# Kernel optimization log

Measured on AMD Instinct MI355X. Metric: run time of the kernel, lower is better.

The kernel has to match this reference:

```python
import jax, jax.numpy as jnp
import numpy as np

DT = 0.001
HIDDEN = 512
OUT = 128

def setup_inputs() -> dict:
    key = jax.random.key(0)
    k1, k2 = jax.random.split(key)
    x = jax.random.normal(k1, (64, 2048, HIDDEN), dtype=jnp.float32)
    # torch Linear default init ~ U(-1/sqrt(fan_in), 1/sqrt(fan_in)), weight shape [out, in]
    lim = 1.0 / np.sqrt(HIDDEN)
    W = jax.random.uniform(k2, (OUT, HIDDEN), dtype=jnp.float32, minval=-lim, maxval=lim)
    tau_syn = jnp.asarray(0.5, dtype=jnp.float32)  # tau_syn_out (used as tau_syn_inv)
    tau_mem = jnp.asarray(0.5, dtype=jnp.float32)  # tau_mem_out (used as tau_mem_inv)
    return {"x": x, "W": W, "tau_syn": tau_syn, "tau_mem": tau_mem}

def reference(x, W, tau_syn, tau_mem):
    # SNNDecode.forward: clamp taus, permute to [seq, batch, in], per-step
    # Linear + norse LI (leaky integrator) feed-forward step with v_leak = 0.
    tau_syn = jnp.clip(tau_syn, 0.0, 1.0)
    tau_mem = jnp.clip(tau_mem, 0.0, 1.0)
    batch, seq, _ = x.shape
    # The per-step Linear is recurrence-independent: hoist it into one big GEMM.
    # z_all: [seq, batch, out]
    z_all = jnp.einsum('bsh,oh->sbo', x, W)
    v0 = jnp.zeros((batch, OUT), dtype=x.dtype)
    i0 = jnp.zeros((batch, OUT), dtype=x.dtype)

    def step(carry, z):
        v, i = carry
        # li_feed_forward_step: dv = dt*tau_mem_inv*((v_leak - v) + i)
        v_new = v + DT * tau_mem * (i - v)
        i_dec = i - DT * tau_syn * i
        i_new = i_dec + z
        return (v_new, i_new), v_new

    (v_f, i_f), voltages = jax.lax.scan(step, (v0, i0), z_all)
    # output stacked over time: [seq, batch, out]; final state (v, i)
    return voltages, v_f, i_f
```

## Files before the change

kernel.cpp:

```cpp
#include <hip/hip_runtime.h>
#include <hip/hip_bf16.h>


typedef __attribute__((ext_vector_type(4))) float          f4;
typedef __attribute__((ext_vector_type(8))) short          s8;
typedef __attribute__((ext_vector_type(4))) unsigned       u4;
typedef __attribute__((ext_vector_type(4))) unsigned short su4;

#define SEQ    2048
#define HID    512
#define CHAINS 8192
#define VOLT   16777216
#define NCH    64
#define CHUNK  32

__device__ __forceinline__ float clamp01(float x) { return fminf(fmaxf(x, 0.f), 1.f); }

__device__ __forceinline__ unsigned pkbf(float x, float y) {
  float2 t; t.x = x; t.y = y;
  union { __hip_bfloat162 h; unsigned u; } c;
  c.h = __float22bfloat162_rn(t);
  return c.u;
}

__device__ __forceinline__ unsigned short f2bf(float f) {
  union { float f; unsigned u; } c; c.f = f;
  unsigned u = c.u;
  unsigned r = (u + 0x7fffu + ((u >> 16) & 1u)) >> 16;
  return (unsigned short)r;
}

__device__ __forceinline__ float bf2f(unsigned short s) {
  union { unsigned u; float f; } c; c.u = ((unsigned)s) << 16; return c.f;
}

__device__ __forceinline__ int swz(int row, int k) {
  return (row * 64 + k) ^ ((row & 7) << 3);
}

__device__ __forceinline__ int zidx(int row, int col) {
  return row * 128 + (col ^ (((row >> 2) & 7) << 4));
}

__global__ __launch_bounds__(256) void k_wconv(const float* __restrict__ W,
                                               unsigned short* __restrict__ Wb) {
  const int i = blockIdx.x * 256 + threadIdx.x;
  const f4 lo = ((const f4*)W)[2 * i];
  const f4 hi = ((const f4*)W)[2 * i + 1];
  su4 v0, v1;
#pragma unroll
  for (int j = 0; j < 4; ++j) { v0[j] = f2bf(lo[j]); v1[j] = f2bf(hi[j]); }
  ((su4*)Wb)[2 * i] = v0;
  ((su4*)Wb)[2 * i + 1] = v1;
}

template <int ZB>
__global__ __launch_bounds__(256, 2) void k_gemm(const float* __restrict__ X,
                                                 const unsigned short* __restrict__ Wb,
                                                 float* __restrict__ Out,
                                                 unsigned short* __restrict__ zbf,
                                                 const float* __restrict__ tau_syn,
                                                 const float* __restrict__ tau_mem,
                                                 float* __restrict__ ws) {
  __shared__ __align__(16) char smem[32768];
  short* const AS           = (short*)smem;
  unsigned short* const ZSb = (unsigned short*)smem;

  const int tid = threadIdx.x;
  const int blk = blockIdx.x;
  const int m0  = blk << 7;
  const int bI  = blk >> 4;
  const int t0  = (blk & 15) << 7;

  const int rbase = tid >> 3;
  const int coff  = (tid & 7) << 3;

  const int lane = tid & 63;
  const int wid  = tid >> 6;
  const int wmb  = (wid >> 1) << 6;
  const int wnb  = (wid & 1) << 6;
  const int lr   = lane & 15;
  const int lk   = (lane >> 4) << 3;

  const float* pX[4];
#pragma unroll
  for (int c = 0; c < 4; ++c)
    pX[c] = X + (size_t)(m0 + (c << 5) + rbase) * HID + coff;
  const unsigned short* pB[4];
#pragma unroll
  for (int ni = 0; ni < 4; ++ni)
    pB[ni] = Wb + (size_t)(wnb + (ni << 4) + lr) * HID + lk;

  f4 acc[4][4];
#pragma unroll
  for (int mi = 0; mi < 4; ++mi)
#pragma unroll
    for (int ni = 0; ni < 4; ++ni) acc[mi][ni] = (f4){0.f, 0.f, 0.f, 0.f};

  f4 xa[3][4][2];
#pragma unroll
  for (int c = 0; c < 4; ++c) {
    xa[0][c][0] = *(const f4*)(pX[c]);
    xa[0][c][1] = *(const f4*)(pX[c] + 4);
    xa[1][c][0] = *(const f4*)(pX[c] + 64);
    xa[1][c][1] = *(const f4*)(pX[c] + 68);
  }

#pragma unroll
  for (int ks = 0; ks < 8; ++ks) {
    const int cur = ks % 3;
    short* const Ac = AS + ((ks & 1) << 13);
#pragma unroll
    for (int c = 0; c < 4; ++c) {
      const int row = (c << 5) + rbase;
      u4 va;
      va[0] = pkbf(xa[cur][c][0][0], xa[cur][c][0][1]);
      va[1] = pkbf(xa[cur][c][0][2], xa[cur][c][0][3]);
      va[2] = pkbf(xa[cur][c][1][0], xa[cur][c][1][1]);
      va[3] = pkbf(xa[cur][c][1][2], xa[cur][c][1][3]);
      *(u4*)&Ac[swz(row, coff)] = va;
    }
    __syncthreads();
    s8 bg[2][4];
#pragma unroll
    for (int kk = 0; kk < 2; ++kk)
#pragma unroll
      for (int ni = 0; ni < 4; ++ni)
        bg[kk][ni] = *(const s8*)(pB[ni] + (ks << 6) + (kk << 5));
    if (ks < 6) {
      const int k0 = (ks + 2) << 6;
      const int nxt = (ks + 2) % 3;
#pragma unroll
      for (int c = 0; c < 4; ++c) {
        xa[nxt][c][0] = *(const f4*)(pX[c] + k0);
        xa[nxt][c][1] = *(const f4*)(pX[c] + k0 + 4);
      }
    }
#pragma unroll
    for (int kk = 0; kk < 2; ++kk) {
      s8 af[4];
#pragma unroll
      for (int mi = 0; mi < 4; ++mi)
        af[mi] = *(const s8*)&Ac[swz(wmb + (mi << 4) + lr, (kk << 5) + lk)];
#pragma unroll
      for (int mi = 0; mi < 4; ++mi)
#pragma unroll
        for (int ni = 0; ni < 4; ++ni)
          acc[mi][ni] = __builtin_amdgcn_mfma_f32_16x16x32_bf16(af[mi], bg[kk][ni],
                                                                acc[mi][ni], 0, 0, 0);
    }
  }

  __syncthreads();
  const int rr = (lane >> 4) << 2;
#pragma unroll
  for (int mi = 0; mi < 4; ++mi)
#pragma unroll
    for (int ni = 0; ni < 4; ++ni)
#pragma unroll
      for (int r = 0; r < 4; ++r)
        ZSb[zidx(wmb + (mi << 4) + rr + r, wnb + (ni << 4) + lr)] =
            f2bf(acc[mi][ni][r]);
  __syncthreads();

#pragma unroll
  for (int i = 0; i < 16; ++i) {
    const int idx  = (i << 8) + tid;
    const int toff = idx >> 5;
    const int c4   = idx & 31;
    const int colp = (c4 << 2) ^ (((toff >> 2) & 7) << 4);
    const su4 zb = *(const su4*)&ZSb[toff * 128 + colp];
    if (ZB) {
      *(su4*)(zbf + (size_t)(t0 + toff) * 8192 + (bI << 7) + (c4 << 2)) = zb;
    } else {
      f4 zf; zf[0] = bf2f(zb[0]); zf[1] = bf2f(zb[1]);
      zf[2] = bf2f(zb[2]); zf[3] = bf2f(zb[3]);
      *(f4*)(Out + (size_t)(t0 + toff) * 8192 + (bI << 7) + (c4 << 2)) = zf;
    }
  }
  {
    const float a  = 0.001f * clamp01(tau_mem[0]);
    const float eb = 1.f - 0.001f * clamp01(tau_syn[0]);
    const int col = tid & 127, h = tid >> 7;
    const int chain = (bI << 7) + col;
#pragma unroll
    for (int s = 0; s < 2; ++s) {
      const int r0 = (h << 6) + (s << 5);
      float v = 0.f, ii = 0.f;
#pragma unroll 8
      for (int j = 0; j < CHUNK; ++j) {
        const float z = bf2f(ZSb[zidx(r0 + j, col)]);
        v  = v + a * (ii - v);
        ii = eb * ii + z;
      }
      const int q = ((blk & 15) << 2) + (h << 1) + s;
      ws[q * CHAINS + chain]                 = v;
      ws[NCH * CHAINS + q * CHAINS + chain]  = ii;
    }
  }
}

__global__ __launch_bounds__(256) void k_comb(const float* __restrict__ tau_syn,
                                              const float* __restrict__ tau_mem,
                                              float* __restrict__ Out,
                                              float* __restrict__ ws) {
  __shared__ __align__(16) f4 SV[NCH][4], SI[NCH][4];
  const int tid = threadIdx.x;
  const int q   = tid >> 2;
  const int s   = tid & 3;
  const int cg  = blockIdx.x * 4 + s;
  const float a  = 0.001f * clamp01(tau_mem[0]);
  const float bb = 0.001f * clamp01(tau_syn[0]);
  const float ea = 1.f - a, eb = 1.f - bb;
  float P = 1.f, Q = 0.f, R = 1.f;
#pragma unroll
  for (int j = 0; j < CHUNK; ++j) { const float Pn = P * ea; Q = P * a + Q * eb; P = Pn; R *= eb; }

  f4* vend = (f4*)ws;
  f4* iend = vend + NCH * 2048;
  f4 xv = vend[q * 2048 + cg];
  f4 xi = iend[q * 2048 + cg];
  SV[q][s] = xv; SI[q][s] = xi;

  float Pd = P, Qd = Q, Rd = R;
#pragma unroll
  for (int d = 1; d < NCH; d <<= 1) {
    __syncthreads();
    f4 av, ai;
    const bool val = (q >= d);
    if (val) { av = SV[q - d][s]; ai = SI[q - d][s]; }
    __syncthreads();
    if (val) {
      xv = xv + Pd * av + Qd * ai;
      xi = xi + Rd * ai;
      SV[q][s] = xv; SI[q][s] = xi;
    }
    const float Pn = Pd * Pd;
    Qd = Pd * Qd + Qd * Rd;
    Pd = Pn;
    Rd = Rd * Rd;
  }
  __syncthreads();
  f4 iv = (f4){0.f, 0.f, 0.f, 0.f}, ij = (f4){0.f, 0.f, 0.f, 0.f};
  if (q > 0) { iv = SV[q - 1][s]; ij = SI[q - 1][s]; }
  vend[q * 2048 + cg] = iv;
  iend[q * 2048 + cg] = ij;
  if (q == NCH - 1) {
    ((f4*)(Out + VOLT))[cg]          = xv;
    ((f4*)(Out + VOLT + CHAINS))[cg] = xi;
  }
}

template <int ZB>
__global__ __launch_bounds__(256) void k_emit(const float* __restrict__ tau_syn,
                                              const float* __restrict__ tau_mem,
                                              float* __restrict__ Out,
                                              const unsigned short* __restrict__ zbf,
                                              const float* __restrict__ ws) {
  const int tid = threadIdx.x;
  const int cg = (blockIdx.x & 31) * 64 + (tid & 63);
  const int q  = (blockIdx.x >> 5) * 4 + (tid >> 6);
  const float a  = 0.001f * clamp01(tau_mem[0]);
  const float eb = 1.f - 0.001f * clamp01(tau_syn[0]);

  const f4* vin = (const f4*)ws;
  const f4* iin = vin + NCH * 2048;
  f4 v  = vin[q * 2048 + cg];
  f4 ii = iin[q * 2048 + cg];

  f4* o4 = (f4*)Out;
  const int tb = q << 5;
#pragma unroll 8
  for (int j = 0; j < CHUNK; ++j) {
    const size_t idx = (size_t)(tb + j) * 2048 + cg;
    f4 z;
    if (ZB) {
      const su4 zb = *(const su4*)(zbf + (((size_t)(tb + j)) << 13) + (cg << 2));
      z[0] = bf2f(zb[0]); z[1] = bf2f(zb[1]); z[2] = bf2f(zb[2]); z[3] = bf2f(zb[3]);
    } else {
      z = o4[idx];
    }
    v  = v + a * (ii - v);
    o4[idx] = v;
    ii = eb * ii + z;
  }
}

extern "C" void kernel_launch(void* const* d_in, const int* in_sizes, int n_in,
                              void* d_out, int out_size, void* d_ws, size_t ws_size,
                              hipStream_t stream) {
  const float* X   = (const float*)d_in[0];
  const float* W   = (const float*)d_in[1];
  const float* tsy = (const float*)d_in[2];
  const float* tme = (const float*)d_in[3];
  float* Out = (float*)d_out;
  float* ws  = (float*)d_ws;
  unsigned short* Wb  = (unsigned short*)((char*)d_ws + (4u << 20));
  unsigned short* zbf = (unsigned short*)((char*)d_ws + (4u << 20) + (128u << 10));
  const size_t need = (4ull << 20) + (128ull << 10) + (32ull << 20);

  k_wconv<<<32, 256, 0, stream>>>(W, Wb);
  if (ws_size >= need) {
    k_gemm<1><<<1024, 256, 0, stream>>>(X, Wb, Out, zbf, tsy, tme, ws);
    k_comb<<<512, 256, 0, stream>>>(tsy, tme, Out, ws);
    k_emit<1><<<512, 256, 0, stream>>>(tsy, tme, Out, zbf, ws);
  } else {
    k_gemm<0><<<1024, 256, 0, stream>>>(X, Wb, Out, zbf, tsy, tme, ws);
    k_comb<<<512, 256, 0, stream>>>(tsy, tme, Out, ws);
    k_emit<0><<<512, 256, 0, stream>>>(tsy, tme, Out, zbf, ws);
  }
}
```

Baseline: 107.4 us.

## Double K-tile depth to 128 with single-stage register prefetch in GEMM

```diff
diff --git a/kernel.cpp b/kernel.cpp
--- a/kernel.cpp
+++ b/kernel.cpp
@@ -34,8 +34,8 @@
   union { unsigned u; float f; } c; c.u = ((unsigned)s) << 16; return c.f;
 }
 
-__device__ __forceinline__ int swz(int row, int k) {
-  return (row * 64 + k) ^ ((row & 7) << 3);
+__device__ __forceinline__ int swz128(int row, int k) {
+  return row * 128 + (k ^ ((row & 7) << 3));
 }
 
 __device__ __forceinline__ int zidx(int row, int col) {
@@ -62,7 +62,7 @@
                                                  const float* __restrict__ tau_syn,
                                                  const float* __restrict__ tau_mem,
                                                  float* __restrict__ ws) {
-  __shared__ __align__(16) char smem[32768];
+  __shared__ __align__(16) char smem[65536];
   short* const AS           = (short*)smem;
   unsigned short* const ZSb = (unsigned short*)smem;
 
@@ -72,8 +72,8 @@
   const int bI  = blk >> 4;
   const int t0  = (blk & 15) << 7;
 
-  const int rbase = tid >> 3;
-  const int coff  = (tid & 7) << 3;
+  const int rbase  = tid >> 3;
+  const int coff16 = (tid & 7) << 4;
 
   const int lane = tid & 63;
   const int wid  = tid >> 6;
@@ -85,7 +85,7 @@
   const float* pX[4];
 #pragma unroll
   for (int c = 0; c < 4; ++c)
-    pX[c] = X + (size_t)(m0 + (c << 5) + rbase) * HID + coff;
+    pX[c] = X + (size_t)(m0 + (c << 5) + rbase) * HID + coff16;
   const unsigned short* pB[4];
 #pragma unroll
   for (int ni = 0; ni < 4; ++ni)
@@ -97,51 +97,51 @@
 #pragma unroll
     for (int ni = 0; ni < 4; ++ni) acc[mi][ni] = (f4){0.f, 0.f, 0.f, 0.f};
 
-  f4 xa[3][4][2];
-#pragma unroll
-  for (int c = 0; c < 4; ++c) {
-    xa[0][c][0] = *(const f4*)(pX[c]);
-    xa[0][c][1] = *(const f4*)(pX[c] + 4);
-    xa[1][c][0] = *(const f4*)(pX[c] + 64);
-    xa[1][c][1] = *(const f4*)(pX[c] + 68);
-  }
-
-#pragma unroll
-  for (int ks = 0; ks < 8; ++ks) {
-    const int cur = ks % 3;
-    short* const Ac = AS + ((ks & 1) << 13);
+  f4 xa[4][4];
+#pragma unroll
+  for (int c = 0; c < 4; ++c)
+#pragma unroll
+    for (int j = 0; j < 4; ++j)
+      xa[c][j] = *(const f4*)(pX[c] + (j << 2));
+
+#pragma unroll
+  for (int ks = 0; ks < 4; ++ks) {
+    short* const Ac = AS + ((ks & 1) << 14);
 #pragma unroll
     for (int c = 0; c < 4; ++c) {
       const int row = (c << 5) + rbase;
-      u4 va;
-      va[0] = pkbf(xa[cur][c][0][0], xa[cur][c][0][1]);
-      va[1] = pkbf(xa[cur][c][0][2], xa[cur][c][0][3]);
-      va[2] = pkbf(xa[cur][c][1][0], xa[cur][c][1][1]);
-      va[3] = pkbf(xa[cur][c][1][2], xa[cur][c][1][3]);
-      *(u4*)&Ac[swz(row, coff)] = va;
+      u4 va, vb;
+      va[0] = pkbf(xa[c][0][0], xa[c][0][1]);
+      va[1] = pkbf(xa[c][0][2], xa[c][0][3]);
+      va[2] = pkbf(xa[c][1][0], xa[c][1][1]);
+      va[3] = pkbf(xa[c][1][2], xa[c][1][3]);
+      vb[0] = pkbf(xa[c][2][0], xa[c][2][1]);
+      vb[1] = pkbf(xa[c][2][2], xa[c][2][3]);
+      vb[2] = pkbf(xa[c][3][0], xa[c][3][1]);
+      vb[3] = pkbf(xa[c][3][2], xa[c][3][3]);
+      *(u4*)&Ac[swz128(row, coff16)]     = va;
+      *(u4*)&Ac[swz128(row, coff16 + 8)] = vb;
     }
     __syncthreads();
-    s8 bg[2][4];
-#pragma unroll
-    for (int kk = 0; kk < 2; ++kk)
+    s8 bg[4][4];
+#pragma unroll
+    for (int kk = 0; kk < 4; ++kk)
 #pragma unroll
       for (int ni = 0; ni < 4; ++ni)
-        bg[kk][ni] = *(const s8*)(pB[ni] + (ks << 6) + (kk << 5));
-    if (ks < 6) {
-      const int k0 = (ks + 2) << 6;
-      const int nxt = (ks + 2) % 3;
-#pragma unroll
-      for (int c = 0; c < 4; ++c) {
-        xa[nxt][c][0] = *(const f4*)(pX[c] + k0);
-        xa[nxt][c][1] = *(const f4*)(pX[c] + k0 + 4);
-      }
-    }
-#pragma unroll
-    for (int kk = 0; kk < 2; ++kk) {
+        bg[kk][ni] = *(const s8*)(pB[ni] + (ks << 7) + (kk << 5));
+    if (ks < 3) {
+#pragma unroll
+      for (int c = 0; c < 4; ++c)
+#pragma unroll
+        for (int j = 0; j < 4; ++j)
+          xa[c][j] = *(const f4*)(pX[c] + ((ks + 1) << 7) + (j << 2));
+    }
+#pragma unroll
+    for (int kk = 0; kk < 4; ++kk) {
       s8 af[4];
 #pragma unroll
       for (int mi = 0; mi < 4; ++mi)
-        af[mi] = *(const s8*)&Ac[swz(wmb + (mi << 4) + lr, (kk << 5) + lk)];
+        af[mi] = *(const s8*)&Ac[swz128(wmb + (mi << 4) + lr, (kk << 5) + lk)];
 #pragma unroll
       for (int mi = 0; mi < 4; ++mi)
 #pragma unroll
```

Measured after the change: 113.5 us. 1.06x slower.

## Stream X tiles directly to LDS with global_load_lds and convert on read

Applied to the files above, without the earlier changes.

```diff
diff --git a/kernel.cpp b/kernel.cpp
--- a/kernel.cpp
+++ b/kernel.cpp
@@ -34,8 +34,10 @@
   union { unsigned u; float f; } c; c.u = ((unsigned)s) << 16; return c.f;
 }
 
-__device__ __forceinline__ int swz(int row, int k) {
-  return (row * 64 + k) ^ ((row & 7) << 3);
+__device__ __forceinline__ void gload16(const float* g, float* l) {
+  __builtin_amdgcn_global_load_lds(
+      (const __attribute__((address_space(1))) void*)g,
+      (__attribute__((address_space(3))) void*)l, 16, 0, 0);
 }
 
 __device__ __forceinline__ int zidx(int row, int col) {
@@ -55,25 +57,21 @@
 }
 
 template <int ZB>
-__global__ __launch_bounds__(256, 2) void k_gemm(const float* __restrict__ X,
+__global__ __launch_bounds__(256, 3) void k_gemm(const float* __restrict__ X,
                                                  const unsigned short* __restrict__ Wb,
                                                  float* __restrict__ Out,
                                                  unsigned short* __restrict__ zbf,
                                                  const float* __restrict__ tau_syn,
                                                  const float* __restrict__ tau_mem,
                                                  float* __restrict__ ws) {
-  __shared__ __align__(16) char smem[32768];
-  short* const AS           = (short*)smem;
-  unsigned short* const ZSb = (unsigned short*)smem;
+  __shared__ __align__(16) float AS[2][128 * 32];
+  unsigned short* const ZSb = (unsigned short*)&AS[0][0];
 
   const int tid = threadIdx.x;
   const int blk = blockIdx.x;
   const int m0  = blk << 7;
   const int bI  = blk >> 4;
   const int t0  = (blk & 15) << 7;
-
-  const int rbase = tid >> 3;
-  const int coff  = (tid & 7) << 3;
 
   const int lane = tid & 63;
   const int wid  = tid >> 6;
@@ -82,10 +80,10 @@
   const int lr   = lane & 15;
   const int lk   = (lane >> 4) << 3;
 
-  const float* pX[4];
-#pragma unroll
-  for (int c = 0; c < 4; ++c)
-    pX[c] = X + (size_t)(m0 + (c << 5) + rbase) * HID + coff;
+  const int srow  = wid << 5;
+  const int lrow8 = lane >> 3;
+  const int lkpos = (lane & 7) << 2;
+
   const unsigned short* pB[4];
 #pragma unroll
   for (int ni = 0; ni < 4; ++ni)
@@ -97,58 +95,54 @@
 #pragma unroll
     for (int ni = 0; ni < 4; ++ni) acc[mi][ni] = (f4){0.f, 0.f, 0.f, 0.f};
 
-  f4 xa[3][4][2];
-#pragma unroll
-  for (int c = 0; c < 4; ++c) {
-    xa[0][c][0] = *(const f4*)(pX[c]);
-    xa[0][c][1] = *(const f4*)(pX[c] + 4);
-    xa[1][c][0] = *(const f4*)(pX[c] + 64);
-    xa[1][c][1] = *(const f4*)(pX[c] + 68);
-  }
-
-#pragma unroll
-  for (int ks = 0; ks < 8; ++ks) {
-    const int cur = ks % 3;
-    short* const Ac = AS + ((ks & 1) << 13);
-#pragma unroll
-    for (int c = 0; c < 4; ++c) {
-      const int row = (c << 5) + rbase;
-      u4 va;
-      va[0] = pkbf(xa[cur][c][0][0], xa[cur][c][0][1]);
-      va[1] = pkbf(xa[cur][c][0][2], xa[cur][c][0][3]);
-      va[2] = pkbf(xa[cur][c][1][0], xa[cur][c][1][1]);
-      va[3] = pkbf(xa[cur][c][1][2], xa[cur][c][1][3]);
-      *(u4*)&Ac[swz(row, coff)] = va;
-    }
+#pragma unroll
+  for (int j = 0; j < 4; ++j) {
+    const int r0  = srow + (j << 3);
+    const int row = r0 + lrow8;
+    const float* src = X + (size_t)(m0 + row) * HID + (lkpos ^ ((row & 7) << 2));
+    gload16(src, &AS[0][r0 * 32]);
+  }
+
+#pragma unroll
+  for (int ks = 0; ks < 16; ++ks) {
+    const float* const Ac = &AS[ks & 1][0];
     __syncthreads();
-    s8 bg[2][4];
-#pragma unroll
-    for (int kk = 0; kk < 2; ++kk)
+    s8 bg[4];
+#pragma unroll
+    for (int ni = 0; ni < 4; ++ni)
+      bg[ni] = *(const s8*)(pB[ni] + (ks << 5));
+    __builtin_amdgcn_sched_barrier(0);
+    if (ks < 15) {
+      float* const An = &AS[(ks + 1) & 1][0];
+      const int kgb = (ks + 1) << 5;
+#pragma unroll
+      for (int j = 0; j < 4; ++j) {
+        const int r0  = srow + (j << 3);
+        const int row = r0 + lrow8;
+        const float* src = X + (size_t)(m0 + row) * HID + kgb +
+                           (lkpos ^ ((row & 7) << 2));
+        gload16(src, An + r0 * 32);
+      }
+    }
+    __builtin_amdgcn_sched_barrier(0);
+    s8 af[4];
+#pragma unroll
+    for (int mi = 0; mi < 4; ++mi) {
+      const int row = wmb + (mi << 4) + lr;
+      const int sw  = (row & 7) << 2;
+      const f4 lo = *(const f4*)&Ac[row * 32 + (lk ^ sw)];
+      const f4 hi = *(const f4*)&Ac[row * 32 + ((lk + 4) ^ sw)];
+      union { u4 u; s8 s; } t;
+      t.u[0] = pkbf(lo[0], lo[1]); t.u[1] = pkbf(lo[2], lo[3]);
+      t.u[2] = pkbf(hi[0], hi[1]); t.u[3] = pkbf(hi[2], hi[3]);
+      af[mi] = t.s;
+    }
+#pragma unroll
+    for (int mi = 0; mi < 4; ++mi)
 #pragma unroll
       for (int ni = 0; ni < 4; ++ni)
-        bg[kk][ni] = *(const s8*)(pB[ni] + (ks << 6) + (kk << 5));
-    if (ks < 6) {
-      const int k0 = (ks + 2) << 6;
-      const int nxt = (ks + 2) % 3;
-#pragma unroll
-      for (int c = 0; c < 4; ++c) {
-        xa[nxt][c][0] = *(const f4*)(pX[c] + k0);
-        xa[nxt][c][1] = *(const f4*)(pX[c] + k0 + 4);
-      }
-    }
-#pragma unroll
-    for (int kk = 0; kk < 2; ++kk) {
-      s8 af[4];
-#pragma unroll
-      for (int mi = 0; mi < 4; ++mi)
-        af[mi] = *(const s8*)&Ac[swz(wmb + (mi << 4) + lr, (kk << 5) + lk)];
-#pragma unroll
-      for (int mi = 0; mi < 4; ++mi)
-#pragma unroll
-        for (int ni = 0; ni < 4; ++ni)
-          acc[mi][ni] = __builtin_amdgcn_mfma_f32_16x16x32_bf16(af[mi], bg[kk][ni],
-                                                                acc[mi][ni], 0, 0, 0);
-    }
+        acc[mi][ni] = __builtin_amdgcn_mfma_f32_16x16x32_bf16(af[mi], bg[ni],
+                                                              acc[mi][ni], 0, 0, 0);
   }
 
   __syncthreads();
```

Measured after the change: 110.1 us. 2.5% more time.
